# Kernel optimization log

Hardware: AMD Instinct MI355X
Metric: run time of the kernel (lower is better)

## Reference

```python
import jax, jax.numpy as jnp
import numpy as np

N, E, D_IN, D_OUT = 50000, 800000, 128, 128


def setup_inputs() -> dict:
    key = jax.random.key(0)
    ks = jax.random.split(key, 16)
    # edges with no self-loops (add_remaining_self_loops then simply appends one loop per node)
    row = jax.random.randint(ks[0], (E,), 0, N, dtype=jnp.int32)
    off = jax.random.randint(ks[1], (E,), 1, N, dtype=jnp.int32)
    col = (row + off) % N
    edge_index = jnp.stack([row, col], axis=0)
    s_in = 1.0 / np.sqrt(D_IN)
    s_out = 1.0 / np.sqrt(D_OUT)
    u = lambda k, shape, s: jax.random.uniform(k, shape, jnp.float32, -s, s)
    return {
        "x": jax.random.normal(ks[2], (N, D_IN), jnp.float32),
        "edge_index": edge_index,
        "W_hp": u(ks[3], (D_OUT, D_IN), s_in), "b_hp": u(ks[4], (D_OUT,), s_in),
        "W_lp": u(ks[5], (D_OUT, D_IN), s_in), "b_lp": u(ks[6], (D_OUT,), s_in),
        "W_i": u(ks[7], (D_OUT, D_IN), s_in), "b_i": u(ks[8], (D_OUT,), s_in),
        "wlin_h": u(ks[9], (D_OUT,), s_out), "blin_h": u(ks[10], (), s_out),
        "wlin_l": u(ks[11], (D_OUT,), s_out), "blin_l": u(ks[12], (), s_out),
        "wlin_i": u(ks[13], (D_OUT,), s_out), "blin_i": u(ks[14], (), s_out),
    }


def reference(x, edge_index, W_hp, b_hp, W_lp, b_lp, W_i, b_i,
              wlin_h, blin_h, wlin_l, blin_l, wlin_i, blin_i):
    n = x.shape[0]
    row, col = edge_index[0], edge_index[1]
    loop = jnp.arange(n, dtype=row.dtype)
    rf = jnp.concatenate([row, loop])  # sources incl. self-loops
    cf = jnp.concatenate([col, loop])  # targets incl. self-loops
    w = jnp.ones(rf.shape[0], x.dtype)
    # symmetric GCN normalization: D^{-1/2} A_hat D^{-1/2}
    deg = jax.ops.segment_sum(w, cf, num_segments=n)
    dinv = jnp.where(deg > 0, deg ** -0.5, 0.0).astype(x.dtype)
    w = dinv[rf] * w * dinv[cf]

    def agg(h):  # out[i] = sum_j w_e * h[j] over edges j->i
        return jax.ops.segment_sum(w[:, None] * h[rf], cf, num_segments=n)

    h_hp = x @ W_hp.T + b_hp
    H_hp = jax.nn.relu(h_hp - agg(h_hp))          # high-pass
    h_lp = x @ W_lp.T + b_lp
    H_lp = jax.nn.relu(agg(h_lp))                 # low-pass
    H_i = jax.nn.relu(x @ W_i.T + b_i)            # identity

    a_h = jax.nn.sigmoid(H_hp @ wlin_h + blin_h)  # [N]
    a_l = jax.nn.sigmoid(H_lp @ wlin_l + blin_l)
    a_i = jax.nn.sigmoid(H_i @ wlin_i + blin_i)
    # diag(alpha) @ H == alpha[:, None] * H
    return a_h[:, None] * H_hp + a_l[:, None] * H_lp + a_i[:, None] * H_i
```

## Files before the change

### kernel.cpp

```cpp
#include <hip/hip_runtime.h>
#include <cstdint>
#include <cstddef>

#define DEV __device__ __forceinline__

typedef __bf16 bf16x8 __attribute__((ext_vector_type(8)));
typedef float f32x4 __attribute__((ext_vector_type(4)));
typedef unsigned short ushort8v __attribute__((ext_vector_type(8)));

DEV ushort f2b(float f) {
  uint u = __float_as_uint(f);
  return (ushort)((u + 0x7FFFu + ((u >> 16) & 1u)) >> 16);
}

DEV float4 shfl_xor4(float4 v, int m) {
  float4 r;
  r.x = __shfl_xor(v.x, m); r.y = __shfl_xor(v.y, m);
  r.z = __shfl_xor(v.z, m); r.w = __shfl_xor(v.w, m);
  return r;
}

DEV float4 unpack4(uint2 u) {
  float4 r;
  r.x = __uint_as_float(u.x << 16);
  r.y = __uint_as_float(u.x & 0xFFFF0000u);
  r.z = __uint_as_float(u.y << 16);
  r.w = __uint_as_float(u.y & 0xFFFF0000u);
  return r;
}

DEV void fma4(float4& a, float w, uint2 u) {
  float4 v = unpack4(u);
  a.x = fmaf(w, v.x, a.x); a.y = fmaf(w, v.y, a.y);
  a.z = fmaf(w, v.z, a.z); a.w = fmaf(w, v.w, a.w);
}

__global__ __launch_bounds__(256) void k_gemm_count(
    const float* __restrict__ x,
    const float* __restrict__ W0, const float* __restrict__ W1,
    const float* __restrict__ W2,
    const float* __restrict__ b_hp, const float* __restrict__ b_lp,
    const float* __restrict__ b_i,
    ushort* __restrict__ h_all, int N,
    const int* __restrict__ col, int* __restrict__ cnt, int E, int nCB) {
  __shared__ ushort Wl[16384];
  int tid = (int)threadIdx.x;
  int bx = (int)blockIdx.x;

  if (bx < nCB) {
    int gsz = nCB * 256;
    for (int e = bx * 256 + tid; e < E; e += gsz)
      atomicAdd(&cnt[col[e]], 1);
    return;
  }
  bx -= nCB;

  int lane = tid & 63, wv = tid >> 6;
  int r = lane & 15, g = lane >> 4;
  int NT = N >> 4;
  int t = bx * 4 + wv;
  bool active = t < NT;

  bf16x8 Af[4];
  if (active) {
    const float* xp = x + ((size_t)t * 16 + r) * 128 + g * 8;
#pragma unroll
    for (int kc = 0; kc < 4; ++kc) {
      float4 v0 = *(const float4*)(xp + kc * 32);
      float4 v1 = *(const float4*)(xp + kc * 32 + 4);
      ushort8v u;
      u[0] = f2b(v0.x); u[1] = f2b(v0.y); u[2] = f2b(v0.z); u[3] = f2b(v0.w);
      u[4] = f2b(v1.x); u[5] = f2b(v1.y); u[6] = f2b(v1.z); u[7] = f2b(v1.w);
      Af[kc] = __builtin_bit_cast(bf16x8, u);
    }
  }

  for (int m = 0; m < 3; ++m) {
    const float* Wsrc = (m == 0) ? W0 : (m == 1) ? W1 : W2;
    __syncthreads();
    for (int i = tid; i < 2048; i += 256) {
      int byte = i << 4;
      int row = byte >> 8;
      int swz = byte ^ ((row & 7) << 4);
      const float* s = Wsrc + (i << 3);
      float4 v0 = *(const float4*)s;
      float4 v1 = *(const float4*)(s + 4);
      ushort8v u;
      u[0] = f2b(v0.x); u[1] = f2b(v0.y); u[2] = f2b(v0.z); u[3] = f2b(v0.w);
      u[4] = f2b(v1.x); u[5] = f2b(v1.y); u[6] = f2b(v1.z); u[7] = f2b(v1.w);
      *(ushort8v*)((char*)Wl + swz) = u;
    }
    __syncthreads();
    if (!active) continue;
    const float* bias = (m == 0) ? b_hp : (m == 1) ? b_lp : b_i;
    f32x4 acc[8];
#pragma unroll
    for (int ct = 0; ct < 8; ++ct) {
      float bb = bias[ct * 16 + r];
      f32x4 c; c[0] = bb; c[1] = bb; c[2] = bb; c[3] = bb;
      acc[ct] = c;
    }
#pragma unroll
    for (int kc = 0; kc < 4; ++kc)
#pragma unroll
      for (int ct = 0; ct < 8; ++ct) {
        int row = ct * 16 + r;
        int byte = row * 256 + kc * 64 + g * 16;
        int swz = byte ^ ((row & 7) << 4);
        bf16x8 B = *(const bf16x8*)((const char*)Wl + swz);
        acc[ct] = __builtin_amdgcn_mfma_f32_16x16x32_bf16(Af[kc], B, acc[ct], 0, 0, 0);
      }
    ushort* op = h_all + (size_t)(t * 16 + g * 4) * 384 + m * 128 + r;
#pragma unroll
    for (int ct = 0; ct < 8; ++ct)
#pragma unroll
      for (int j = 0; j < 4; ++j) {
        float v = acc[ct][j];
        if (m == 2) v = fmaxf(v, 0.f);
        op[(size_t)j * 384 + ct * 16] = f2b(v);
      }
  }
}

__global__ __launch_bounds__(256) void k_scanA(const int* __restrict__ cnt,
                                               int* __restrict__ off,
                                               float* __restrict__ dinv,
                                               int* __restrict__ btot, int N) {
  __shared__ int ws[4];
  int t = threadIdx.x, ln = t & 63, wv = t >> 6;
  int i = blockIdx.x * 256 + t;
  int v = (i < N) ? cnt[i] : 0;
  int inc = v;
#pragma unroll
  for (int o = 1; o < 64; o <<= 1) {
    int u = __shfl_up(inc, o);
    if (ln >= o) inc += u;
  }
  if (ln == 63) ws[wv] = inc;
  __syncthreads();
  if (t == 0) {
    int s = 0;
#pragma unroll
    for (int w = 0; w < 4; ++w) { int tmp = ws[w]; ws[w] = s; s += tmp; }
  }
  __syncthreads();
  int excl = ws[wv] + inc - v;
  if (i < N) {
    off[i] = excl;
    dinv[i] = rsqrtf((float)v + 1.0f);
  }
  if (t == 255) btot[blockIdx.x] = excl + v;
}

__global__ __launch_bounds__(256) void k_scanBC(int* __restrict__ off,
                                                const int* __restrict__ btot,
                                                int* __restrict__ cursor,
                                                int N, int E, int NB) {
  __shared__ int ws[4];
  __shared__ int pre_sh[256];
  int t = threadIdx.x, ln = t & 63, wv = t >> 6;
  int v = (t < NB) ? btot[t] : 0;
  int inc = v;
#pragma unroll
  for (int o = 1; o < 64; o <<= 1) {
    int u = __shfl_up(inc, o);
    if (ln >= o) inc += u;
  }
  if (ln == 63) ws[wv] = inc;
  __syncthreads();
  if (t == 0) {
    int s = 0;
#pragma unroll
    for (int w = 0; w < 4; ++w) { int tmp = ws[w]; ws[w] = s; s += tmp; }
  }
  __syncthreads();
  pre_sh[t] = ws[wv] + inc - v;
  __syncthreads();
  int bpre = pre_sh[blockIdx.x];
  int i = blockIdx.x * 256 + t;
  if (i < N) {
    int o = off[i] + bpre;
    off[i] = o;
    cursor[i] = o;
  }
  if (blockIdx.x == 0 && t == 0) off[N] = E;
}

__global__ __launch_bounds__(256) void k_scatter(const int* __restrict__ ei,
                                                 const float* __restrict__ dinv,
                                                 int* __restrict__ cursor,
                                                 int2* __restrict__ edata, int E) {
  int e = blockIdx.x * 256 + threadIdx.x;
  if (e >= E) return;
  int s = ei[e], d = ei[E + e];
  float ws = dinv[s];
  int p = atomicAdd(&cursor[d], 1);
  int2 v; v.x = s; v.y = __float_as_int(ws);
  edata[p] = v;
}

__global__ __launch_bounds__(256) void k_agg_final(
    const ushort* __restrict__ h_all, const float* __restrict__ dinv,
    const int* __restrict__ off, const int2* __restrict__ edata,
    const float* __restrict__ wlh, const float* __restrict__ wll,
    const float* __restrict__ wli,
    const float* __restrict__ pbh, const float* __restrict__ pbl,
    const float* __restrict__ pbi,
    float* __restrict__ out, int N) {
  int wv = __builtin_amdgcn_readfirstlane((int)threadIdx.x >> 6);
  int lane = (int)threadIdx.x & 63;
  int node = blockIdx.x * 4 + wv;
  if (node >= N) return;

  const ushort* hb = h_all + 4 * lane;
  int p0 = off[node], p1 = off[node + 1];

  float4 a0 = {0,0,0,0}, a1 = {0,0,0,0}, a2 = {0,0,0,0}, a3 = {0,0,0,0};
  float4 a4 = {0,0,0,0}, a5 = {0,0,0,0}, a6 = {0,0,0,0}, a7 = {0,0,0,0};
  int p = p0;
  for (; p + 8 <= p1; p += 8) {
    int2 e0 = edata[p],     e1 = edata[p + 1], e2 = edata[p + 2], e3 = edata[p + 3];
    int2 e4 = edata[p + 4], e5 = edata[p + 5], e6 = edata[p + 6], e7 = edata[p + 7];
    uint2 u0 = *(const uint2*)(const void*)(hb + (size_t)e0.x * 384);
    uint2 u1 = *(const uint2*)(const void*)(hb + (size_t)e1.x * 384);
    uint2 u2 = *(const uint2*)(const void*)(hb + (size_t)e2.x * 384);
    uint2 u3 = *(const uint2*)(const void*)(hb + (size_t)e3.x * 384);
    uint2 u4 = *(const uint2*)(const void*)(hb + (size_t)e4.x * 384);
    uint2 u5 = *(const uint2*)(const void*)(hb + (size_t)e5.x * 384);
    uint2 u6 = *(const uint2*)(const void*)(hb + (size_t)e6.x * 384);
    uint2 u7 = *(const uint2*)(const void*)(hb + (size_t)e7.x * 384);
    fma4(a0, __int_as_float(e0.y), u0);
    fma4(a1, __int_as_float(e1.y), u1);
    fma4(a2, __int_as_float(e2.y), u2);
    fma4(a3, __int_as_float(e3.y), u3);
    fma4(a4, __int_as_float(e4.y), u4);
    fma4(a5, __int_as_float(e5.y), u5);
    fma4(a6, __int_as_float(e6.y), u6);
    fma4(a7, __int_as_float(e7.y), u7);
  }
  for (; p < p1; ++p) {
    int2 e = edata[p];
    uint2 u = *(const uint2*)(const void*)(hb + (size_t)e.x * 384);
    fma4(a0, __int_as_float(e.y), u);
  }
  float4 own;
  own.x = ((a0.x + a1.x) + (a2.x + a3.x)) + ((a4.x + a5.x) + (a6.x + a7.x));
  own.y = ((a0.y + a1.y) + (a2.y + a3.y)) + ((a4.y + a5.y) + (a6.y + a7.y));
  own.z = ((a0.z + a1.z) + (a2.z + a3.z)) + ((a4.z + a5.z) + (a6.z + a7.z));
  own.w = ((a0.w + a1.w) + (a2.w + a3.w)) + ((a4.w + a5.w) + (a6.w + a7.w));

  float di = dinv[node];
  float4 sv = unpack4(*(const uint2*)(const void*)(hb + (size_t)node * 384));
  own.x = (own.x + di * sv.x) * di; own.y = (own.y + di * sv.y) * di;
  own.z = (own.z + di * sv.z) * di; own.w = (own.w + di * sv.w) * di;

  float4 oth = shfl_xor4(own, 32);
  float4 svo = shfl_xor4(sv, 32);
  bool hpside = (lane < 32);
  float4 hpSelf, aggHp, aggLp;
  hpSelf.x = hpside ? sv.x : svo.x; hpSelf.y = hpside ? sv.y : svo.y;
  hpSelf.z = hpside ? sv.z : svo.z; hpSelf.w = hpside ? sv.w : svo.w;
  aggHp.x = hpside ? own.x : oth.x; aggHp.y = hpside ? own.y : oth.y;
  aggHp.z = hpside ? own.z : oth.z; aggHp.w = hpside ? own.w : oth.w;
  aggLp.x = hpside ? oth.x : own.x; aggLp.y = hpside ? oth.y : own.y;
  aggLp.z = hpside ? oth.z : own.z; aggLp.w = hpside ? oth.w : own.w;

  float4 Hh, Hl;
  Hh.x = fmaxf(hpSelf.x - aggHp.x, 0.f); Hh.y = fmaxf(hpSelf.y - aggHp.y, 0.f);
  Hh.z = fmaxf(hpSelf.z - aggHp.z, 0.f); Hh.w = fmaxf(hpSelf.w - aggHp.w, 0.f);
  Hl.x = fmaxf(aggLp.x, 0.f); Hl.y = fmaxf(aggLp.y, 0.f);
  Hl.z = fmaxf(aggLp.z, 0.f); Hl.w = fmaxf(aggLp.w, 0.f);

  int c4 = 4 * (lane & 31);
  float4 hi4 = unpack4(*(const uint2*)(const void*)(h_all + (size_t)node * 384 + 256 + c4));
  float4 wh = *(const float4*)(wlh + c4);
  float4 wl = *(const float4*)(wll + c4);
  float4 wi = *(const float4*)(wli + c4);

  float dh = Hh.x * wh.x + Hh.y * wh.y + Hh.z * wh.z + Hh.w * wh.w;
  float dl = Hl.x * wl.x + Hl.y * wl.y + Hl.z * wl.z + Hl.w * wl.w;
  float dd = hi4.x * wi.x + hi4.y * wi.y + hi4.z * wi.z + hi4.w * wi.w;
#pragma unroll
  for (int o = 32; o > 0; o >>= 1) {
    dh += __shfl_xor(dh, o);
    dl += __shfl_xor(dl, o);
    dd += __shfl_xor(dd, o);
  }
  float a_h = 1.f / (1.f + __expf(-(0.5f * dh + pbh[0])));
  float a_l = 1.f / (1.f + __expf(-(0.5f * dl + pbl[0])));
  float a_i = 1.f / (1.f + __expf(-(0.5f * dd + pbi[0])));

  if (hpside) {
    float4 o4;
    o4.x = a_h * Hh.x + a_l * Hl.x + a_i * hi4.x;
    o4.y = a_h * Hh.y + a_l * Hl.y + a_i * hi4.y;
    o4.z = a_h * Hh.z + a_l * Hl.z + a_i * hi4.z;
    o4.w = a_h * Hh.w + a_l * Hl.w + a_i * hi4.w;
    *(float4*)(out + (size_t)node * 128 + c4) = o4;
  }
}

extern "C" void kernel_launch(void* const* d_in, const int* in_sizes, int n_in,
                              void* d_out, int out_size, void* d_ws, size_t ws_size,
                              hipStream_t stream) {
  const float* x     = (const float*)d_in[0];
  const int*   ei    = (const int*)d_in[1];
  const float* W_hp  = (const float*)d_in[2];
  const float* b_hp  = (const float*)d_in[3];
  const float* W_lp  = (const float*)d_in[4];
  const float* b_lp  = (const float*)d_in[5];
  const float* W_i   = (const float*)d_in[6];
  const float* b_i   = (const float*)d_in[7];
  const float* wlh   = (const float*)d_in[8];
  const float* pbh   = (const float*)d_in[9];
  const float* wll   = (const float*)d_in[10];
  const float* pbl   = (const float*)d_in[11];
  const float* wli   = (const float*)d_in[12];
  const float* pbi   = (const float*)d_in[13];
  float* out = (float*)d_out;

  int N = in_sizes[0] / 128;
  int E = in_sizes[1] / 2;
  int NB = (N + 255) / 256;

  ushort* h_all = (ushort*)d_ws;
  int2*   edata = (int2*)(h_all + (size_t)N * 384);
  float*  dinv  = (float*)(edata + E);
  int*    cnt   = (int*)(dinv + N);
  int*    off   = cnt + N;
  int*    cursor= off + N + 1;
  int*    btot  = cursor + N;

  int nGB = (N / 16 + 3) / 4;
  int nCB = 782;

  hipMemsetAsync(cnt, 0, sizeof(int) * N, stream);
  k_gemm_count<<<nCB + nGB, 256, 0, stream>>>(
      x, W_hp, W_lp, W_i, b_hp, b_lp, b_i, h_all, N, ei + E, cnt, E, nCB);
  k_scanA<<<NB, 256, 0, stream>>>(cnt, off, dinv, btot, N);
  k_scanBC<<<NB, 256, 0, stream>>>(off, btot, cursor, N, E, NB);
  k_scatter<<<(E + 255) / 256, 256, 0, stream>>>(ei, dinv, cursor, edata, E);
  k_agg_final<<<(N + 3) / 4, 256, 0, stream>>>(
      h_all, dinv, off, edata, wlh, wll, wli, pbh, pbl, pbi, out, N);
}
```

Before: 271.0 us.

## Aggregate input features before the projection GEMM and fuse the epilogue into it

Uses the linearity of the aggregation to gather 128-wide bf16 rows of x instead of 256-wide projected hidden rows. The bias is carried through a per-node sum of edge weights, and the high-pass input becomes x minus agg(x). A new fused kernel then runs the three MFMA GEMMs with relu, the gating dot products, the sigmoids and the weighted combine, writing the output directly. This is meant to halve the gather traffic and drop the intermediate hidden-buffer round trip. In exchange it adds an fp32 aggregated-x buffer written and read back, a separate x-to-bf16 conversion pass, and holds three accumulator sets in registers, which may lower occupancy.

```diff
diff --git a/kernel.cpp b/kernel.cpp
--- a/kernel.cpp
+++ b/kernel.cpp
@@ -12,66 +12,229 @@
   uint u = __float_as_uint(f);
   return (ushort)((u + 0x7FFFu + ((u >> 16) & 1u)) >> 16);
 }
-
-DEV float4 shfl_xor4(float4 v, int m) {
-  float4 r;
-  r.x = __shfl_xor(v.x, m); r.y = __shfl_xor(v.y, m);
-  r.z = __shfl_xor(v.z, m); r.w = __shfl_xor(v.w, m);
-  return r;
-}
-
-DEV float4 unpack4(uint2 u) {
-  float4 r;
-  r.x = __uint_as_float(u.x << 16);
-  r.y = __uint_as_float(u.x & 0xFFFF0000u);
-  r.z = __uint_as_float(u.y << 16);
-  r.w = __uint_as_float(u.y & 0xFFFF0000u);
-  return r;
-}
-
-DEV void fma4(float4& a, float w, uint2 u) {
-  float4 v = unpack4(u);
-  a.x = fmaf(w, v.x, a.x); a.y = fmaf(w, v.y, a.y);
-  a.z = fmaf(w, v.z, a.z); a.w = fmaf(w, v.w, a.w);
-}
-
-__global__ __launch_bounds__(256) void k_gemm_count(
-    const float* __restrict__ x,
+DEV float bf_lo(uint u) { return __uint_as_float(u << 16); }
+DEV float bf_hi(uint u) { return __uint_as_float(u & 0xFFFF0000u); }
+
+__global__ __launch_bounds__(256) void k_cvt_count(
+    const float* __restrict__ x, ushort* __restrict__ xb, int n8,
+    const int* __restrict__ col, int* __restrict__ cnt, int E, int nCV) {
+  int b = (int)blockIdx.x, tid = (int)threadIdx.x;
+  if (b < nCV) {
+    int gsz = nCV * 256;
+    for (int i = b * 256 + tid; i < n8; i += gsz) {
+      const float* s = x + (size_t)i * 8;
+      float4 v0 = *(const float4*)s;
+      float4 v1 = *(const float4*)(s + 4);
+      ushort8v u;
+      u[0] = f2b(v0.x); u[1] = f2b(v0.y); u[2] = f2b(v0.z); u[3] = f2b(v0.w);
+      u[4] = f2b(v1.x); u[5] = f2b(v1.y); u[6] = f2b(v1.z); u[7] = f2b(v1.w);
+      *(ushort8v*)(xb + (size_t)i * 8) = u;
+    }
+    return;
+  }
+  b -= nCV;
+  int e = b * 256 + tid;
+  if (e < E) atomicAdd(&cnt[col[e]], 1);
+}
+
+__global__ __launch_bounds__(256) void k_scanA(const int* __restrict__ cnt,
+                                               int* __restrict__ off,
+                                               float* __restrict__ dinv,
+                                               int* __restrict__ btot, int N) {
+  __shared__ int ws[4];
+  int t = threadIdx.x, ln = t & 63, wv = t >> 6;
+  int i = blockIdx.x * 256 + t;
+  int v = (i < N) ? cnt[i] : 0;
+  int inc = v;
+#pragma unroll
+  for (int o = 1; o < 64; o <<= 1) {
+    int u = __shfl_up(inc, o);
+    if (ln >= o) inc += u;
+  }
+  if (ln == 63) ws[wv] = inc;
+  __syncthreads();
+  if (t == 0) {
+    int s = 0;
+#pragma unroll
+    for (int w = 0; w < 4; ++w) { int tmp = ws[w]; ws[w] = s; s += tmp; }
+  }
+  __syncthreads();
+  int excl = ws[wv] + inc - v;
+  if (i < N) {
+    off[i] = excl;
+    dinv[i] = rsqrtf((float)v + 1.0f);
+  }
+  if (t == 255) btot[blockIdx.x] = excl + v;
+}
+
+__global__ __launch_bounds__(256) void k_scanBC(int* __restrict__ off,
+                                                const int* __restrict__ btot,
+                                                int* __restrict__ cursor,
+                                                int N, int E, int NB) {
+  __shared__ int ws[4];
+  __shared__ int pre_sh[256];
+  int t = threadIdx.x, ln = t & 63, wv = t >> 6;
+  int v = (t < NB) ? btot[t] : 0;
+  int inc = v;
+#pragma unroll
+  for (int o = 1; o < 64; o <<= 1) {
+    int u = __shfl_up(inc, o);
+    if (ln >= o) inc += u;
+  }
+  if (ln == 63) ws[wv] = inc;
+  __syncthreads();
+  if (t == 0) {
+    int s = 0;
+#pragma unroll
+    for (int w = 0; w < 4; ++w) { int tmp = ws[w]; ws[w] = s; s += tmp; }
+  }
+  __syncthreads();
+  pre_sh[t] = ws[wv] + inc - v;
+  __syncthreads();
+  int bpre = pre_sh[blockIdx.x];
+  int i = blockIdx.x * 256 + t;
+  if (i < N) {
+    int o = off[i] + bpre;
+    off[i] = o;
+    cursor[i] = o;
+  }
+  if (blockIdx.x == 0 && t == 0) off[N] = E;
+}
+
+__global__ __launch_bounds__(256) void k_scatter(const int* __restrict__ ei,
+                                                 const float* __restrict__ dinv,
+                                                 int* __restrict__ cursor,
+                                                 int2* __restrict__ edata, int E) {
+  int e = blockIdx.x * 256 + threadIdx.x;
+  if (e >= E) return;
+  int s = ei[e], d = ei[E + e];
+  float ws = dinv[s];
+  int p = atomicAdd(&cursor[d], 1);
+  int2 v; v.x = s; v.y = __float_as_int(ws);
+  edata[p] = v;
+}
+
+__global__ __launch_bounds__(256) void k_agg_x(
+    const ushort* __restrict__ xb, const float* __restrict__ dinv,
+    const int* __restrict__ off, const int2* __restrict__ edata,
+    float* __restrict__ xa, float* __restrict__ sarr, int N) {
+  int wv = __builtin_amdgcn_readfirstlane((int)threadIdx.x >> 6);
+  int lane = (int)threadIdx.x & 63;
+  int node = blockIdx.x * 4 + wv;
+  if (node >= N) return;
+
+  const ushort* gb = xb + 2 * lane;
+  int p0 = off[node], p1 = off[node + 1];
+
+  float2 a0 = {0,0}, a1 = {0,0}, a2 = {0,0}, a3 = {0,0};
+  float2 a4 = {0,0}, a5 = {0,0}, a6 = {0,0}, a7 = {0,0};
+  float sd = 0.f;
+  int p = p0;
+  for (; p + 8 <= p1; p += 8) {
+    int2 e0 = edata[p],     e1 = edata[p + 1], e2 = edata[p + 2], e3 = edata[p + 3];
+    int2 e4 = edata[p + 4], e5 = edata[p + 5], e6 = edata[p + 6], e7 = edata[p + 7];
+    uint u0 = *(const uint*)(const void*)(gb + (size_t)e0.x * 128);
+    uint u1 = *(const uint*)(const void*)(gb + (size_t)e1.x * 128);
+    uint u2 = *(const uint*)(const void*)(gb + (size_t)e2.x * 128);
+    uint u3 = *(const uint*)(const void*)(gb + (size_t)e3.x * 128);
+    uint u4 = *(const uint*)(const void*)(gb + (size_t)e4.x * 128);
+    uint u5 = *(const uint*)(const void*)(gb + (size_t)e5.x * 128);
+    uint u6 = *(const uint*)(const void*)(gb + (size_t)e6.x * 128);
+    uint u7 = *(const uint*)(const void*)(gb + (size_t)e7.x * 128);
+    float w0 = __int_as_float(e0.y), w1 = __int_as_float(e1.y);
+    float w2 = __int_as_float(e2.y), w3 = __int_as_float(e3.y);
+    float w4 = __int_as_float(e4.y), w5 = __int_as_float(e5.y);
+    float w6 = __int_as_float(e6.y), w7 = __int_as_float(e7.y);
+    a0.x = fmaf(w0, bf_lo(u0), a0.x); a0.y = fmaf(w0, bf_hi(u0), a0.y);
+    a1.x = fmaf(w1, bf_lo(u1), a1.x); a1.y = fmaf(w1, bf_hi(u1), a1.y);
+    a2.x = fmaf(w2, bf_lo(u2), a2.x); a2.y = fmaf(w2, bf_hi(u2), a2.y);
+    a3.x = fmaf(w3, bf_lo(u3), a3.x); a3.y = fmaf(w3, bf_hi(u3), a3.y);
+    a4.x = fmaf(w4, bf_lo(u4), a4.x); a4.y = fmaf(w4, bf_hi(u4), a4.y);
+    a5.x = fmaf(w5, bf_lo(u5), a5.x); a5.y = fmaf(w5, bf_hi(u5), a5.y);
+    a6.x = fmaf(w6, bf_lo(u6), a6.x); a6.y = fmaf(w6, bf_hi(u6), a6.y);
+    a7.x = fmaf(w7, bf_lo(u7), a7.x); a7.y = fmaf(w7, bf_hi(u7), a7.y);
+    sd += ((w0 + w1) + (w2 + w3)) + ((w4 + w5) + (w6 + w7));
+  }
+  for (; p < p1; ++p) {
+    int2 e = edata[p];
+    uint u = *(const uint*)(const void*)(gb + (size_t)e.x * 128);
+    float w = __int_as_float(e.y);
+    a0.x = fmaf(w, bf_lo(u), a0.x); a0.y = fmaf(w, bf_hi(u), a0.y);
+    sd += w;
+  }
+  float ax = ((a0.x + a1.x) + (a2.x + a3.x)) + ((a4.x + a5.x) + (a6.x + a7.x));
+  float ay = ((a0.y + a1.y) + (a2.y + a3.y)) + ((a4.y + a5.y) + (a6.y + a7.y));
+
+  float di = dinv[node];
+  uint us = *(const uint*)(const void*)(gb + (size_t)node * 128);
+  ax = (ax + di * bf_lo(us)) * di;
+  ay = (ay + di * bf_hi(us)) * di;
+  float si = (sd + di) * di;
+
+  float2 st; st.x = ax; st.y = ay;
+  *(float2*)(xa + (size_t)node * 128 + 2 * lane) = st;
+  if (lane == 0) sarr[node] = si;
+}
+
+__global__ __launch_bounds__(256) void k_mega(
+    const float* __restrict__ x, const float* __restrict__ xa,
+    const float* __restrict__ sarr,
     const float* __restrict__ W0, const float* __restrict__ W1,
     const float* __restrict__ W2,
     const float* __restrict__ b_hp, const float* __restrict__ b_lp,
     const float* __restrict__ b_i,
-    ushort* __restrict__ h_all, int N,
-    const int* __restrict__ col, int* __restrict__ cnt, int E, int nCB) {
+    const float* __restrict__ wlh, const float* __restrict__ wll,
+    const float* __restrict__ wli,
+    const float* __restrict__ pbh, const float* __restrict__ pbl,
+    const float* __restrict__ pbi,
+    float* __restrict__ out, int N) {
   __shared__ ushort Wl[16384];
   int tid = (int)threadIdx.x;
-  int bx = (int)blockIdx.x;
-
-  if (bx < nCB) {
-    int gsz = nCB * 256;
-    for (int e = bx * 256 + tid; e < E; e += gsz)
-      atomicAdd(&cnt[col[e]], 1);
-    return;
-  }
-  bx -= nCB;
-
   int lane = tid & 63, wv = tid >> 6;
   int r = lane & 15, g = lane >> 4;
   int NT = N >> 4;
-  int t = bx * 4 + wv;
+  int t = (int)blockIdx.x * 4 + wv;
   bool active = t < NT;
 
-  bf16x8 Af[4];
+  bf16x8 Ax[4], Ad[4], Aa[4];
+  float sj[4];
   if (active) {
     const float* xp = x + ((size_t)t * 16 + r) * 128 + g * 8;
+    const float* ap = xa + ((size_t)t * 16 + r) * 128 + g * 8;
 #pragma unroll
     for (int kc = 0; kc < 4; ++kc) {
       float4 v0 = *(const float4*)(xp + kc * 32);
       float4 v1 = *(const float4*)(xp + kc * 32 + 4);
-      ushort8v u;
-      u[0] = f2b(v0.x); u[1] = f2b(v0.y); u[2] = f2b(v0.z); u[3] = f2b(v0.w);
-      u[4] = f2b(v1.x); u[5] = f2b(v1.y); u[6] = f2b(v1.z); u[7] = f2b(v1.w);
-      Af[kc] = __builtin_bit_cast(bf16x8, u);
+      float4 w0 = *(const float4*)(ap + kc * 32);
+      float4 w1 = *(const float4*)(ap + kc * 32 + 4);
+      ushort8v ux, ud, ua;
+      ux[0] = f2b(v0.x); ux[1] = f2b(v0.y); ux[2] = f2b(v0.z); ux[3] = f2b(v0.w);
+      ux[4] = f2b(v1.x); ux[5] = f2b(v1.y); ux[6] = f2b(v1.z); ux[7] = f2b(v1.w);
+      ud[0] = f2b(v0.x - w0.x); ud[1] = f2b(v0.y - w0.y);
+      ud[2] = f2b(v0.z - w0.z); ud[3] = f2b(v0.w - w0.w);
+      ud[4] = f2b(v1.x - w1.x); ud[5] = f2b(v1.y - w1.y);
+      ud[6] = f2b(v1.z - w1.z); ud[7] = f2b(v1.w - w1.w);
+      ua[0] = f2b(w0.x); ua[1] = f2b(w0.y); ua[2] = f2b(w0.z); ua[3] = f2b(w0.w);
+      ua[4] = f2b(w1.x); ua[5] = f2b(w1.y); ua[6] = f2b(w1.z); ua[7] = f2b(w1.w);
+      Ax[kc] = __builtin_bit_cast(bf16x8, ux);
+      Ad[kc] = __builtin_bit_cast(bf16x8, ud);
+      Aa[kc] = __builtin_bit_cast(bf16x8, ua);
+    }
+#pragma unroll
+    for (int j = 0; j < 4; ++j) sj[j] = sarr[t * 16 + 4 * g + j];
+  }
+
+  f32x4 aH[8], aL[8], aI[8];
+  if (active) {
+#pragma unroll
+    for (int ct = 0; ct < 8; ++ct) {
+      float bh = b_hp[ct * 16 + r], bl = b_lp[ct * 16 + r], bi = b_i[ct * 16 + r];
+#pragma unroll
+      for (int j = 0; j < 4; ++j) {
+        aH[ct][j] = (1.f - sj[j]) * bh;
+        aL[ct][j] = sj[j] * bl;
+        aI[ct][j] = bi;
+      }
     }
   }
 
@@ -92,14 +255,6 @@
     }
     __syncthreads();
     if (!active) continue;
-    const float* bias = (m == 0) ? b_hp : (m == 1) ? b_lp : b_i;
-    f32x4 acc[8];
-#pragma unroll
-    for (int ct = 0; ct < 8; ++ct) {
-      float bb = bias[ct * 16 + r];
-      f32x4 c; c[0] = bb; c[1] = bb; c[2] = bb; c[3] = bb;
-      acc[ct] = c;
-    }
 #pragma unroll
     for (int kc = 0; kc < 4; ++kc)
 #pragma unroll
@@ -108,196 +263,52 @@
         int byte = row * 256 + kc * 64 + g * 16;
         int swz = byte ^ ((row & 7) << 4);
         bf16x8 B = *(const bf16x8*)((const char*)Wl + swz);
-        acc[ct] = __builtin_amdgcn_mfma_f32_16x16x32_bf16(Af[kc], B, acc[ct], 0, 0, 0);
+        if (m == 0)      aH[ct] = __builtin_amdgcn_mfma_f32_16x16x32_bf16(Ad[kc], B, aH[ct], 0, 0, 0);
+        else if (m == 1) aL[ct] = __builtin_amdgcn_mfma_f32_16x16x32_bf16(Aa[kc], B, aL[ct], 0, 0, 0);
+        else             aI[ct] = __builtin_amdgcn_mfma_f32_16x16x32_bf16(Ax[kc], B, aI[ct], 0, 0, 0);
       }
-    ushort* op = h_all + (size_t)(t * 16 + g * 4) * 384 + m * 128 + r;
-#pragma unroll
-    for (int ct = 0; ct < 8; ++ct)
-#pragma unroll
-      for (int j = 0; j < 4; ++j) {
-        float v = acc[ct][j];
-        if (m == 2) v = fmaxf(v, 0.f);
-        op[(size_t)j * 384 + ct * 16] = f2b(v);
-      }
-  }
-}
-
-__global__ __launch_bounds__(256) void k_scanA(const int* __restrict__ cnt,
-                                               int* __restrict__ off,
-                                               float* __restrict__ dinv,
-                                               int* __restrict__ btot, int N) {
-  __shared__ int ws[4];
-  int t = threadIdx.x, ln = t & 63, wv = t >> 6;
-  int i = blockIdx.x * 256 + t;
-  int v = (i < N) ? cnt[i] : 0;
-  int inc = v;
-#pragma unroll
-  for (int o = 1; o < 64; o <<= 1) {
-    int u = __shfl_up(inc, o);
-    if (ln >= o) inc += u;
-  }
-  if (ln == 63) ws[wv] = inc;
-  __syncthreads();
-  if (t == 0) {
-    int s = 0;
-#pragma unroll
-    for (int w = 0; w < 4; ++w) { int tmp = ws[w]; ws[w] = s; s += tmp; }
-  }
-  __syncthreads();
-  int excl = ws[wv] + inc - v;
-  if (i < N) {
-    off[i] = excl;
-    dinv[i] = rsqrtf((float)v + 1.0f);
-  }
-  if (t == 255) btot[blockIdx.x] = excl + v;
-}
-
-__global__ __launch_bounds__(256) void k_scanBC(int* __restrict__ off,
-                                                const int* __restrict__ btot,
-                                                int* __restrict__ cursor,
-                                                int N, int E, int NB) {
-  __shared__ int ws[4];
-  __shared__ int pre_sh[256];
-  int t = threadIdx.x, ln = t & 63, wv = t >> 6;
-  int v = (t < NB) ? btot[t] : 0;
-  int inc = v;
-#pragma unroll
-  for (int o = 1; o < 64; o <<= 1) {
-    int u = __shfl_up(inc, o);
-    if (ln >= o) inc += u;
-  }
-  if (ln == 63) ws[wv] = inc;
-  __syncthreads();
-  if (t == 0) {
-    int s = 0;
-#pragma unroll
-    for (int w = 0; w < 4; ++w) { int tmp = ws[w]; ws[w] = s; s += tmp; }
-  }
-  __syncthreads();
-  pre_sh[t] = ws[wv] + inc - v;
-  __syncthreads();
-  int bpre = pre_sh[blockIdx.x];
-  int i = blockIdx.x * 256 + t;
-  if (i < N) {
-    int o = off[i] + bpre;
-    off[i] = o;
-    cursor[i] = o;
-  }
-  if (blockIdx.x == 0 && t == 0) off[N] = E;
-}
-
-__global__ __launch_bounds__(256) void k_scatter(const int* __restrict__ ei,
-                                                 const float* __restrict__ dinv,
-                                                 int* __restrict__ cursor,
-                                                 int2* __restrict__ edata, int E) {
-  int e = blockIdx.x * 256 + threadIdx.x;
-  if (e >= E) return;
-  int s = ei[e], d = ei[E + e];
-  float ws = dinv[s];
-  int p = atomicAdd(&cursor[d], 1);
-  int2 v; v.x = s; v.y = __float_as_int(ws);
-  edata[p] = v;
-}
-
-__global__ __launch_bounds__(256) void k_agg_final(
-    const ushort* __restrict__ h_all, const float* __restrict__ dinv,
-    const int* __restrict__ off, const int2* __restrict__ edata,
-    const float* __restrict__ wlh, const float* __restrict__ wll,
-    const float* __restrict__ wli,
-    const float* __restrict__ pbh, const float* __restrict__ pbl,
-    const float* __restrict__ pbi,
-    float* __restrict__ out, int N) {
-  int wv = __builtin_amdgcn_readfirstlane((int)threadIdx.x >> 6);
-  int lane = (int)threadIdx.x & 63;
-  int node = blockIdx.x * 4 + wv;
-  if (node >= N) return;
-
-  const ushort* hb = h_all + 4 * lane;
-  int p0 = off[node], p1 = off[node + 1];
-
-  float4 a0 = {0,0,0,0}, a1 = {0,0,0,0}, a2 = {0,0,0,0}, a3 = {0,0,0,0};
-  float4 a4 = {0,0,0,0}, a5 = {0,0,0,0}, a6 = {0,0,0,0}, a7 = {0,0,0,0};
-  int p = p0;
-  for (; p + 8 <= p1; p += 8) {
-    int2 e0 = edata[p],     e1 = edata[p + 1], e2 = edata[p + 2], e3 = edata[p + 3];
-    int2 e4 = edata[p + 4], e5 = edata[p + 5], e6 = edata[p + 6], e7 = edata[p + 7];
-    uint2 u0 = *(const uint2*)(const void*)(hb + (size_t)e0.x * 384);
-    uint2 u1 = *(const uint2*)(const void*)(hb + (size_t)e1.x * 384);
-    uint2 u2 = *(const uint2*)(const void*)(hb + (size_t)e2.x * 384);
-    uint2 u3 = *(const uint2*)(const void*)(hb + (size_t)e3.x * 384);
-    uint2 u4 = *(const uint2*)(const void*)(hb + (size_t)e4.x * 384);
-    uint2 u5 = *(const uint2*)(const void*)(hb + (size_t)e5.x * 384);
-    uint2 u6 = *(const uint2*)(const void*)(hb + (size_t)e6.x * 384);
-    uint2 u7 = *(const uint2*)(const void*)(hb + (size_t)e7.x * 384);
-    fma4(a0, __int_as_float(e0.y), u0);
-    fma4(a1, __int_as_float(e1.y), u1);
-    fma4(a2, __int_as_float(e2.y), u2);
-    fma4(a3, __int_as_float(e3.y), u3);
-    fma4(a4, __int_as_float(e4.y), u4);
-    fma4(a5, __int_as_float(e5.y), u5);
-    fma4(a6, __int_as_float(e6.y), u6);
-    fma4(a7, __int_as_float(e7.y), u7);
-  }
-  for (; p < p1; ++p) {
-    int2 e = edata[p];
-    uint2 u = *(const uint2*)(const void*)(hb + (size_t)e.x * 384);
-    fma4(a0, __int_as_float(e.y), u);
-  }
-  float4 own;
-  own.x = ((a0.x + a1.x) + (a2.x + a3.x)) + ((a4.x + a5.x) + (a6.x + a7.x));
-  own.y = ((a0.y + a1.y) + (a2.y + a3.y)) + ((a4.y + a5.y) + (a6.y + a7.y));
-  own.z = ((a0.z + a1.z) + (a2.z + a3.z)) + ((a4.z + a5.z) + (a6.z + a7.z));
-  own.w = ((a0.w + a1.w) + (a2.w + a3.w)) + ((a4.w + a5.w) + (a6.w + a7.w));
-
-  float di = dinv[node];
-  float4 sv = unpack4(*(const uint2*)(const void*)(hb + (size_t)node * 384));
-  own.x = (own.x + di * sv.x) * di; own.y = (own.y + di * sv.y) * di;
-  own.z = (own.z + di * sv.z) * di; own.w = (own.w + di * sv.w) * di;
-
-  float4 oth = shfl_xor4(own, 32);
-  float4 svo = shfl_xor4(sv, 32);
-  bool hpside = (lane < 32);
-  float4 hpSelf, aggHp, aggLp;
-  hpSelf.x = hpside ? sv.x : svo.x; hpSelf.y = hpside ? sv.y : svo.y;
-  hpSelf.z = hpside ? sv.z : svo.z; hpSelf.w = hpside ? sv.w : svo.w;
-  aggHp.x = hpside ? own.x : oth.x; aggHp.y = hpside ? own.y : oth.y;
-  aggHp.z = hpside ? own.z : oth.z; aggHp.w = hpside ? own.w : oth.w;
-  aggLp.x = hpside ? oth.x : own.x; aggLp.y = hpside ? oth.y : own.y;
-  aggLp.z = hpside ? oth.z : own.z; aggLp.w = hpside ? oth.w : own.w;
-
-  float4 Hh, Hl;
-  Hh.x = fmaxf(hpSelf.x - aggHp.x, 0.f); Hh.y = fmaxf(hpSelf.y - aggHp.y, 0.f);
-  Hh.z = fmaxf(hpSelf.z - aggHp.z, 0.f); Hh.w = fmaxf(hpSelf.w - aggHp.w, 0.f);
-  Hl.x = fmaxf(aggLp.x, 0.f); Hl.y = fmaxf(aggLp.y, 0.f);
-  Hl.z = fmaxf(aggLp.z, 0.f); Hl.w = fmaxf(aggLp.w, 0.f);
-
-  int c4 = 4 * (lane & 31);
-  float4 hi4 = unpack4(*(const uint2*)(const void*)(h_all + (size_t)node * 384 + 256 + c4));
-  float4 wh = *(const float4*)(wlh + c4);
-  float4 wl = *(const float4*)(wll + c4);
-  float4 wi = *(const float4*)(wli + c4);
-
-  float dh = Hh.x * wh.x + Hh.y * wh.y + Hh.z * wh.z + Hh.w * wh.w;
-  float dl = Hl.x * wl.x + Hl.y * wl.y + Hl.z * wl.z + Hl.w * wl.w;
-  float dd = hi4.x * wi.x + hi4.y * wi.y + hi4.z * wi.z + hi4.w * wi.w;
-#pragma unroll
-  for (int o = 32; o > 0; o >>= 1) {
-    dh += __shfl_xor(dh, o);
-    dl += __shfl_xor(dl, o);
-    dd += __shfl_xor(dd, o);
-  }
-  float a_h = 1.f / (1.f + __expf(-(0.5f * dh + pbh[0])));
-  float a_l = 1.f / (1.f + __expf(-(0.5f * dl + pbl[0])));
-  float a_i = 1.f / (1.f + __expf(-(0.5f * dd + pbi[0])));
-
-  if (hpside) {
-    float4 o4;
-    o4.x = a_h * Hh.x + a_l * Hl.x + a_i * hi4.x;
-    o4.y = a_h * Hh.y + a_l * Hl.y + a_i * hi4.y;
-    o4.z = a_h * Hh.z + a_l * Hl.z + a_i * hi4.z;
-    o4.w = a_h * Hh.w + a_l * Hl.w + a_i * hi4.w;
-    *(float4*)(out + (size_t)node * 128 + c4) = o4;
-  }
+  }
+  if (!active) return;
+
+  float dh[4] = {0,0,0,0}, dl[4] = {0,0,0,0}, dd[4] = {0,0,0,0};
+#pragma unroll
+  for (int ct = 0; ct < 8; ++ct) {
+    float wh = wlh[ct * 16 + r], wl = wll[ct * 16 + r], wi = wli[ct * 16 + r];
+#pragma unroll
+    for (int j = 0; j < 4; ++j) {
+      float Hh = fmaxf(aH[ct][j], 0.f);
+      float Hl = fmaxf(aL[ct][j], 0.f);
+      float Hi = fmaxf(aI[ct][j], 0.f);
+      aH[ct][j] = Hh; aL[ct][j] = Hl; aI[ct][j] = Hi;
+      dh[j] = fmaf(Hh, wh, dh[j]);
+      dl[j] = fmaf(Hl, wl, dl[j]);
+      dd[j] = fmaf(Hi, wi, dd[j]);
+    }
+  }
+#pragma unroll
+  for (int o = 1; o <= 8; o <<= 1) {
+#pragma unroll
+    for (int j = 0; j < 4; ++j) {
+      dh[j] += __shfl_xor(dh[j], o);
+      dl[j] += __shfl_xor(dl[j], o);
+      dd[j] += __shfl_xor(dd[j], o);
+    }
+  }
+  float bh0 = pbh[0], bl0 = pbl[0], bi0 = pbi[0];
+  float ah[4], al[4], ai[4];
+#pragma unroll
+  for (int j = 0; j < 4; ++j) {
+    ah[j] = 1.f / (1.f + __expf(-(dh[j] + bh0)));
+    al[j] = 1.f / (1.f + __expf(-(dl[j] + bl0)));
+    ai[j] = 1.f / (1.f + __expf(-(dd[j] + bi0)));
+  }
+#pragma unroll
+  for (int ct = 0; ct < 8; ++ct)
+#pragma unroll
+    for (int j = 0; j < 4; ++j) {
+      float v = ah[j] * aH[ct][j] + al[j] * aL[ct][j] + ai[j] * aI[ct][j];
+      out[(size_t)(t * 16 + 4 * g + j) * 128 + ct * 16 + r] = v;
+    }
 }
 
 extern "C" void kernel_launch(void* const* d_in, const int* in_sizes, int n_in,
@@ -323,23 +334,26 @@
   int E = in_sizes[1] / 2;
   int NB = (N + 255) / 256;
 
-  ushort* h_all = (ushort*)d_ws;
-  int2*   edata = (int2*)(h_all + (size_t)N * 384);
+  ushort* xb    = (ushort*)d_ws;
+  float*  xa    = (float*)(xb + (size_t)N * 128);
+  float*  sarr  = xa + (size_t)N * 128;
+  int2*   edata = (int2*)(sarr + N);
   float*  dinv  = (float*)(edata + E);
   int*    cnt   = (int*)(dinv + N);
   int*    off   = cnt + N;
   int*    cursor= off + N + 1;
   int*    btot  = cursor + N;
 
-  int nGB = (N / 16 + 3) / 4;
-  int nCB = 782;
+  int nCV = 512;
 
   hipMemsetAsync(cnt, 0, sizeof(int) * N, stream);
-  k_gemm_count<<<nCB + nGB, 256, 0, stream>>>(
-      x, W_hp, W_lp, W_i, b_hp, b_lp, b_i, h_all, N, ei + E, cnt, E, nCB);
+  k_cvt_count<<<nCV + (E + 255) / 256, 256, 0, stream>>>(
+      x, xb, N * 16, ei + E, cnt, E, nCV);
   k_scanA<<<NB, 256, 0, stream>>>(cnt, off, dinv, btot, N);
   k_scanBC<<<NB, 256, 0, stream>>>(off, btot, cursor, N, E, NB);
   k_scatter<<<(E + 255) / 256, 256, 0, stream>>>(ei, dinv, cursor, edata, E);
-  k_agg_final<<<(N + 3) / 4, 256, 0, stream>>>(
-      h_all, dinv, off, edata, wlh, wll, wli, pbh, pbl, pbi, out, N);
-}
+  k_agg_x<<<(N + 3) / 4, 256, 0, stream>>>(xb, dinv, off, edata, xa, sarr, N);
+  k_mega<<<(N / 16 + 3) / 4, 256, 0, stream>>>(
+      x, xa, sarr, W_hp, W_lp, W_i, b_hp, b_lp, b_i,
+      wlh, wll, wli, pbh, pbl, pbi, out, N);
+}
```

After: 277.7 us. 1.02x slower.
